# Kernel tuning notes

Hardware: AMD Instinct MI355X
Metric: run time of the kernel (lower is better)

The kernel has to match this reference:

```python
import jax, jax.numpy as jnp
import numpy as np

T = 4.0          # kd_T
PATCH_NUM = 16
MASK_NUM = 4
P = PATCH_NUM - MASK_NUM  # 12
B = 4096
D_IN = 640
D = 128


def embed(x, w1, b1, w2, b2):
    # Linear -> ReLU -> Linear -> L2 normalize over features
    h = jax.nn.relu(x @ w1.T + b1)
    y = h @ w2.T + b2
    norm = jnp.sqrt(jnp.sum(y * y, axis=1, keepdims=True))
    return y / norm


def kl_rows(y_s, y_t):
    # Matches KLDiv: kl_div(log_softmax(y_s/T), softmax(y_t/T), 'batchmean') * T^2
    # over dim=0 of a 1-D vector -> sum / D. Vectorized over leading dims.
    ls = jax.nn.log_softmax(y_s / T, axis=-1)
    lt = jax.nn.log_softmax(y_t / T, axis=-1)
    pt = jnp.exp(lt)
    return jnp.sum(pt * (lt - ls), axis=-1) / y_s.shape[-1] * (T * T)


def setup_inputs() -> dict:
    key = jax.random.key(0)
    ks = jax.random.split(key, 11)
    return {
        "ebg": jax.random.normal(ks[0], (B, D_IN), jnp.float32),
        "ebp": jax.random.normal(ks[1], (P * B, D_IN), jnp.float32),
        "labelsg": jax.random.randint(ks[2], (B,), 0, 64),
        "glo_w1": jax.random.normal(ks[3], (D, D_IN), jnp.float32) * 0.04,
        "glo_b1": jax.random.normal(ks[4], (D,), jnp.float32) * 0.02,
        "glo_w2": jax.random.normal(ks[5], (D, D), jnp.float32) * 0.09,
        "glo_b2": jax.random.normal(ks[6], (D,), jnp.float32) * 0.02,
        "pat_w1": jax.random.normal(ks[7], (D, D_IN), jnp.float32) * 0.04,
        "pat_b1": jax.random.normal(ks[8], (D,), jnp.float32) * 0.02,
        "pat_w2": jax.random.normal(ks[9], (D, D), jnp.float32) * 0.09,
        "pat_b2": jax.random.normal(ks[10], (D,), jnp.float32) * 0.02,
    }


def reference(ebg, ebp, labelsg, glo_w1, glo_b1, glo_w2, glo_b2,
              pat_w1, pat_b1, pat_w2, pat_b2):
    sg = jax.lax.stop_gradient
    g = embed(ebg, glo_w1, glo_b1, glo_w2, glo_b2)          # [B, D]
    p = embed(ebp, pat_w1, pat_b1, pat_w2, pat_b2)          # [P*B, D]
    p = p.reshape(P, B, D)
    p_bar = p.mean(axis=0)                                  # [B, D]

    # soft_dil_loss: symmetric KL between g[b] and p_bar[b]
    dil = jnp.sum(kl_rows(g, sg(p_bar)) + kl_rows(p_bar, sg(g)))

    # soft_dcl_loss: symmetric KL between (g[b]-p[b,l])^2 and (p_bar[b]-p[b,l])^2
    p_bt = jnp.transpose(p, (1, 0, 2))                      # [B, P, D]
    d1 = (g[:, None, :] - p_bt) ** 2                        # [B, P, D]
    d2 = (p_bar[:, None, :] - p_bt) ** 2                    # [B, P, D]
    dcl = jnp.sum(kl_rows(d1, sg(d2)) + kl_rows(d2, sg(d1))) / P

    return (dil, dcl)
```

## Files before the change

### kernel.cpp

```cpp
#include <hip/hip_runtime.h>
#include <math.h>

#define B_    4096
#define DIN   640
#define DD    128
#define PP    12
#define INV_T 0.25f

typedef __bf16 bft;
typedef __attribute__((ext_vector_type(8))) __bf16 bf16x8;
typedef __attribute__((ext_vector_type(4))) float fx4;

__device__ __forceinline__ void gload16(const float* gp, float* lp) {
  __builtin_amdgcn_global_load_lds(
      (const __attribute__((address_space(1))) unsigned int*)gp,
      (__attribute__((address_space(3))) unsigned int*)lp,
      16, 0, 0);
}

__global__ __launch_bounds__(256) void prep_kernel(
    const float* __restrict__ gw1, const float* __restrict__ pw1,
    const float* __restrict__ gw2, const float* __restrict__ pw2,
    bft* __restrict__ w1fg, bft* __restrict__ w1fp,
    bft* __restrict__ w2fg, bft* __restrict__ w2fp)
{
  int id = blockIdx.x * 256 + threadIdx.x;
  const float* src;
  bft* dst;
  int nt, kc, hl, lane, kstride;
  if (id < 40960) {
    const bool isg = (id < 20480);
    int f = isg ? id : (id - 20480);
    src = isg ? gw1 : pw1;
    dst = isg ? w1fg : w1fp;
    lane = f & 63;
    int q2 = f >> 6;
    hl = q2 & 1;
    int q3 = q2 >> 1;
    kc = q3 % 20; nt = q3 / 20;
    kstride = DIN;
    dst += ((size_t)(nt * 20 + kc) * 2 + hl) * 512 + lane * 8;
  } else {
    const bool isg = (id < 45056);
    int f = isg ? (id - 40960) : (id - 45056);
    src = isg ? gw2 : pw2;
    dst = isg ? w2fg : w2fp;
    lane = f & 63;
    int q2 = f >> 6;
    hl = q2 & 1;
    int q3 = q2 >> 1;
    kc = q3 & 3; nt = q3 >> 2;
    kstride = DD;
    dst += ((size_t)(nt * 4 + kc) * 2 + hl) * 512 + lane * 8;
  }
  int ln = lane & 15, quad = lane >> 4;
  const float* s = src + (size_t)(nt * 16 + ln) * kstride + kc * 32 + quad * 8;
#pragma unroll
  for (int e = 0; e < 8; e++) {
    float x = s[e];
    bft h = (bft)x;
    dst[e] = hl ? (bft)(x - (float)h) : h;
  }
}

__global__ __launch_bounds__(256, 2) void embed_kernel(
    const float* __restrict__ ebg, const float* __restrict__ ebp,
    const bft* __restrict__ w1fg, const float* __restrict__ b1g,
    const bft* __restrict__ w2fg, const float* __restrict__ b2g,
    const bft* __restrict__ w1fp, const float* __restrict__ b1p,
    const bft* __restrict__ w2fp, const float* __restrict__ b2p,
    float* __restrict__ outg, float* __restrict__ outp)
{
  __shared__ __align__(16) bft hsm[2 * 128 * 128];
  float* xbase = (float*)hsm;
  bft* hhi = hsm;
  bft* hlo = hsm + 128 * 128;
  float* halfsq = (float*)hsm;

  const int t = threadIdx.x;
  const int w = t >> 6, lane = t & 63;
  const int wm = w >> 1, wn = w & 1;
  const int ln = lane & 15, quad = lane >> 4;

  const float *X, *B1, *B2;
  const bft *W1F, *W2F;
  float* Y;
  long m0;
  const bool isg = (blockIdx.x < 32);
  if (isg) {
    X = ebg; W1F = w1fg; B1 = b1g; W2F = w2fg; B2 = b2g;
    Y = outg; m0 = (long)blockIdx.x * 128;
  } else {
    X = ebp; W1F = w1fp; B1 = b1p; W2F = w2fp; B2 = b2p;
    Y = outp; m0 = (long)(blockIdx.x - 32) * 128;
  }

  const int srow = lane >> 3;
  const int skq  = (lane & 7) ^ srow;
  const float* xsrc = X + (size_t)(m0 + w * 32 + srow) * DIN + skq * 4;
  const int ldst = w * 32 * 32 + lane * 4;

#define GLX(bufp, k0)                                        \
  _Pragma("unroll")                                          \
  for (int j = 0; j < 4; j++)                                \
    gload16(xsrc + (size_t)j * 8 * DIN + (k0), (bufp) + ldst + j * 8 * 32);

  const int s0 = ((quad << 1) ^ (ln & 7));

  const bft* p1f[4];
#pragma unroll
  for (int nt = 0; nt < 4; nt++)
    p1f[nt] = W1F + (size_t)(wn * 4 + nt) * 20480 + lane * 8;

  fx4 acc[4][4];
#pragma unroll
  for (int mt = 0; mt < 4; mt++)
#pragma unroll
    for (int nt = 0; nt < 4; nt++) acc[mt][nt] = (fx4){0.f, 0.f, 0.f, 0.f};

#define LOADW(wh, wl, kcv)                                 \
  _Pragma("unroll")                                        \
  for (int nt = 0; nt < 4; nt++) {                         \
    wh[nt] = *(const bf16x8*)(p1f[nt] + (kcv) * 1024);     \
    wl[nt] = *(const bf16x8*)(p1f[nt] + (kcv) * 1024 + 512); \
  }

#define PH1CHUNK(bufp, wh, wl)                                                         \
  {                                                                                    \
    bf16x8 ah[4], al[4];                                                               \
    _Pragma("unroll")                                                                  \
    for (int mt = 0; mt < 4; mt++) {                                                   \
      const float* rp = (bufp) + (wm * 64 + mt * 16 + ln) * 32;                        \
      fx4 x0 = *(const fx4*)(rp + s0 * 4);                                             \
      fx4 x1 = *(const fx4*)(rp + (s0 ^ 1) * 4);                                       \
      _Pragma("unroll")                                                                \
      for (int j = 0; j < 4; j++) {                                                    \
        float xv = x0[j];                                                              \
        bft hh = (bft)xv;                                                              \
        ah[mt][j] = hh;                                                                \
        al[mt][j] = (bft)(xv - (float)hh);                                             \
        float yv = x1[j];                                                              \
        bft hh2 = (bft)yv;                                                             \
        ah[mt][4 + j] = hh2;                                                           \
        al[mt][4 + j] = (bft)(yv - (float)hh2);                                        \
      }                                                                                \
    }                                                                                  \
    _Pragma("unroll")                                                                  \
    for (int mt = 0; mt < 4; mt++)                                                     \
      _Pragma("unroll")                                                                \
      for (int nt = 0; nt < 4; nt++) {                                                 \
        acc[mt][nt] = __builtin_amdgcn_mfma_f32_16x16x32_bf16(ah[mt], wh[nt], acc[mt][nt], 0, 0, 0); \
        acc[mt][nt] = __builtin_amdgcn_mfma_f32_16x16x32_bf16(al[mt], wh[nt], acc[mt][nt], 0, 0, 0); \
        acc[mt][nt] = __builtin_amdgcn_mfma_f32_16x16x32_bf16(ah[mt], wl[nt], acc[mt][nt], 0, 0, 0); \
      }                                                                                \
  }

  bf16x8 wha[4], wla[4], whb[4], wlb[4];
  GLX(xbase, 0)
  GLX(xbase + 4096, 32)
  GLX(xbase + 8192, 64)
  LOADW(wha, wla, 0)

#define HALFSTEP(c, WCH, WCL, WNH, WNL, VMTOK)                              \
  {                                                                          \
    const int kn_ = ((c) + 1 < 20) ? ((c) + 1) : 0;                          \
    LOADW(WNH, WNL, kn_)                                                     \
    asm volatile("s_waitcnt vmcnt(" VMTOK ") lgkmcnt(0)" ::: "memory");      \
    __builtin_amdgcn_s_barrier();                                            \
    __builtin_amdgcn_sched_barrier(0);                                       \
    const int kp_ = ((c) + 3 < 20) ? ((c) + 3) * 32 : 0;                     \
    float* pslot_ = xbase + ((((c) + 3) & 3) << 12);                         \
    GLX(pslot_, kp_)                                                         \
    PH1CHUNK(xbase + ((((c) & 3)) << 12), WCH, WCL)                          \
  }

  HALFSTEP(0, wha, wla, whb, wlb, "24")
  for (int kc = 1; kc < 19; kc += 2) {
    HALFSTEP(kc,     whb, wlb, wha, wla, "32")
    HALFSTEP(kc + 1, wha, wla, whb, wlb, "32")
  }
  HALFSTEP(19, whb, wlb, wha, wla, "32")

  __syncthreads();

#pragma unroll
  for (int nt = 0; nt < 4; nt++) {
    float bv = B1[wn * 64 + nt * 16 + ln];
    int c8 = wn * 8 + nt * 2 + (ln >> 3);
    int c7 = ln & 7;
#pragma unroll
    for (int mt = 0; mt < 4; mt++) {
#pragma unroll
      for (int r = 0; r < 4; r++) {
        float v = fmaxf(acc[mt][nt][r] + bv, 0.f);
        bft h = (bft)v;
        bft l = (bft)(v - (float)h);
        int m = wm * 64 + mt * 16 + quad * 4 + r;
        int addr = m * 128 + ((c8 ^ (m & 15)) << 3) + c7;
        hhi[addr] = h;
        hlo[addr] = l;
      }
    }
  }

  const bft* p2f[4];
#pragma unroll
  for (int nt = 0; nt < 4; nt++)
    p2f[nt] = W2F + (size_t)(wn * 4 + nt) * 4096 + lane * 8;

  fx4 acc2[4][4];
#pragma unroll
  for (int nt = 0; nt < 4; nt++) {
    float bv = B2[wn * 64 + nt * 16 + ln];
#pragma unroll
    for (int mt = 0; mt < 4; mt++) acc2[mt][nt] = (fx4){bv, bv, bv, bv};
  }

#define LOADW2(wh, wl, kcv)                                \
  _Pragma("unroll")                                        \
  for (int nt = 0; nt < 4; nt++) {                         \
    wh[nt] = *(const bf16x8*)(p2f[nt] + (kcv) * 1024);     \
    wl[nt] = *(const bf16x8*)(p2f[nt] + (kcv) * 1024 + 512); \
  }

#define PH2CHUNK(kcv, wh, wl)                                                          \
  {                                                                                    \
    bf16x8 ah2[4], al2[4];                                                             \
    _Pragma("unroll")                                                                  \
    for (int mt = 0; mt < 4; mt++) {                                                   \
      int m = wm * 64 + mt * 16 + ln;                                                  \
      int c8 = ((kcv) * 4 + quad) ^ (m & 15);                                          \
      ah2[mt] = *(const bf16x8*)&hhi[m * 128 + (c8 << 3)];                             \
      al2[mt] = *(const bf16x8*)&hlo[m * 128 + (c8 << 3)];                             \
    }                                                                                  \
    _Pragma("unroll")                                                                  \
    for (int mt = 0; mt < 4; mt++)                                                     \
      _Pragma("unroll")                                                                \
      for (int nt = 0; nt < 4; nt++) {                                                 \
        acc2[mt][nt] = __builtin_amdgcn_mfma_f32_16x16x32_bf16(ah2[mt], wh[nt], acc2[mt][nt], 0, 0, 0); \
        acc2[mt][nt] = __builtin_amdgcn_mfma_f32_16x16x32_bf16(al2[mt], wh[nt], acc2[mt][nt], 0, 0, 0); \
        acc2[mt][nt] = __builtin_amdgcn_mfma_f32_16x16x32_bf16(ah2[mt], wl[nt], acc2[mt][nt], 0, 0, 0); \
      }                                                                                \
  }

  bf16x8 q2ha[4], q2la[4], q2hb[4], q2lb[4];
  LOADW2(q2ha, q2la, 0)
  __syncthreads();
  LOADW2(q2hb, q2lb, 1)
  PH2CHUNK(0, q2ha, q2la)
  LOADW2(q2ha, q2la, 2)
  PH2CHUNK(1, q2hb, q2lb)
  LOADW2(q2hb, q2lb, 3)
  PH2CHUNK(2, q2ha, q2la)
  PH2CHUNK(3, q2hb, q2lb)
  __syncthreads();

#pragma unroll
  for (int mt = 0; mt < 4; mt++) {
#pragma unroll
    for (int r = 0; r < 4; r++) {
      float s = 0.f;
#pragma unroll
      for (int nt = 0; nt < 4; nt++) { float v = acc2[mt][nt][r]; s += v * v; }
      s += __shfl_xor(s, 1, 64);
      s += __shfl_xor(s, 2, 64);
      s += __shfl_xor(s, 4, 64);
      s += __shfl_xor(s, 8, 64);
      if (ln == 0) halfsq[(wm * 64 + mt * 16 + quad * 4 + r) * 2 + wn] = s;
    }
  }
  __syncthreads();
#pragma unroll
  for (int mt = 0; mt < 4; mt++) {
#pragma unroll
    for (int r = 0; r < 4; r++) {
      int row = wm * 64 + mt * 16 + quad * 4 + r;
      float rinv = 1.0f / sqrtf(halfsq[row * 2] + halfsq[row * 2 + 1]);
      long R = m0 + row;
#pragma unroll
      for (int nt = 0; nt < 4; nt++) {
        float val = acc2[mt][nt][r] * rinv;
        int col = wn * 64 + nt * 16 + ln;
        if (isg) {
          Y[R * DD + col] = val;
        } else {
          long l_ = R >> 12, b_ = R & 4095;
          Y[(b_ * PP + l_) * DD + col] = val;
        }
      }
    }
  }
}

__device__ __forceinline__ float sym_kl_row(float au0, float au1, float av0, float av1)
{
  float eu0 = __expf(au0), eu1 = __expf(au1);
  float ev0 = __expf(av0), ev1 = __expf(av1);
  float su = eu0 + eu1, sv = ev0 + ev1;
#pragma unroll
  for (int o = 32; o > 0; o >>= 1) {
    su += __shfl_xor(su, o, 64);
    sv += __shfl_xor(sv, o, 64);
  }
  float ru = 1.0f / su, rv = 1.0f / sv;
  float d0 = au0 - av0, d1 = au1 - av1;
  float part = (eu0 * ru - ev0 * rv) * d0 + (eu1 * ru - ev1 * rv) * d1;
#pragma unroll
  for (int o = 32; o > 0; o >>= 1) part += __shfl_xor(part, o, 64);
  return part;
}

__global__ __launch_bounds__(256) void loss_kernel(
    const float* __restrict__ g, const float* __restrict__ p,
    float* __restrict__ pdil, float* __restrict__ pdcl)
{
  __shared__ float wd[4], wc[4];
  int w = threadIdx.x >> 6, lane = threadIdx.x & 63;
  int b = blockIdx.x * 4 + w;
  float2 pl[PP];
  float sx = 0.f, sy = 0.f;
#pragma unroll
  for (int l = 0; l < PP; l++) {
    pl[l] = *(const float2*)&p[((size_t)b * PP + l) * DD + lane * 2];
    sx += pl[l].x; sy += pl[l].y;
  }
  sx *= (1.0f / PP); sy *= (1.0f / PP);
  float2 gv = *(const float2*)&g[(size_t)b * DD + lane * 2];

  float dil = sym_kl_row(gv.x * INV_T, gv.y * INV_T, sx * INV_T, sy * INV_T) * 0.125f;

  float dcl = 0.f;
#pragma unroll
  for (int l = 0; l < PP; l++) {
    float u0 = (gv.x - pl[l].x) * (gv.x - pl[l].x) * INV_T;
    float u1 = (gv.y - pl[l].y) * (gv.y - pl[l].y) * INV_T;
    float v0 = (sx - pl[l].x) * (sx - pl[l].x) * INV_T;
    float v1 = (sy - pl[l].y) * (sy - pl[l].y) * INV_T;
    dcl += sym_kl_row(u0, u1, v0, v1);
  }
  dcl *= (1.0f / 96.0f);

  if (lane == 0) { wd[w] = dil; wc[w] = dcl; }
  __syncthreads();
  if (threadIdx.x == 0) pdil[blockIdx.x] = wd[0] + wd[1] + wd[2] + wd[3];
  if (threadIdx.x == 1) pdcl[blockIdx.x] = wc[0] + wc[1] + wc[2] + wc[3];
}

__global__ __launch_bounds__(256) void final_kernel(const float* __restrict__ pdil,
                                                    const float* __restrict__ pdcl,
                                                    float* __restrict__ out)
{
  __shared__ float red[8];
  int t = threadIdx.x;
  float s0 = 0.f, s1 = 0.f;
  for (int i = t; i < 1024; i += 256) { s0 += pdil[i]; s1 += pdcl[i]; }
#pragma unroll
  for (int o = 32; o > 0; o >>= 1) {
    s0 += __shfl_xor(s0, o, 64);
    s1 += __shfl_xor(s1, o, 64);
  }
  int wid = t >> 6, lane = t & 63;
  if (lane == 0) { red[wid] = s0; red[4 + wid] = s1; }
  __syncthreads();
  if (t == 0) out[0] = red[0] + red[1] + red[2] + red[3];
  if (t == 1) out[1] = red[4] + red[5] + red[6] + red[7];
}

extern "C" void kernel_launch(void* const* d_in, const int* in_sizes, int n_in,
                              void* d_out, int out_size, void* d_ws, size_t ws_size,
                              hipStream_t stream)
{
  const float* ebg = (const float*)d_in[0];
  const float* ebp = (const float*)d_in[1];
  const float* gw1 = (const float*)d_in[3];
  const float* gb1 = (const float*)d_in[4];
  const float* gw2 = (const float*)d_in[5];
  const float* gb2 = (const float*)d_in[6];
  const float* pw1 = (const float*)d_in[7];
  const float* pb1 = (const float*)d_in[8];
  const float* pw2 = (const float*)d_in[9];
  const float* pb2 = (const float*)d_in[10];
  float* out = (float*)d_out;

  float* ws   = (float*)d_ws;
  float* g    = ws;
  float* p    = g + (size_t)B_ * DD;
  float* pdil = p + (size_t)PP * B_ * DD;
  float* pdcl = pdil + 1024;
  bft* wb   = (bft*)(pdcl + 1024);
  bft* w1fg = wb;
  bft* w1fp = w1fg + 163840;
  bft* w2fg = w1fp + 163840;
  bft* w2fp = w2fg + 32768;

  prep_kernel<<<192, 256, 0, stream>>>(gw1, pw1, gw2, pw2,
                                       w1fg, w1fp, w2fg, w2fp);
  embed_kernel<<<416, 256, 0, stream>>>(ebg, ebp,
                                        w1fg, gb1, w2fg, gb2,
                                        w1fp, pb1, w2fp, pb2,
                                        g, p);
  loss_kernel<<<B_ / 4, 256, 0, stream>>>(g, p, pdil, pdcl);
  final_kernel<<<1, 256, 0, stream>>>(pdil, pdcl, out);
}
```

Measured before the change: 246.0 us.

## Give each wave private X staging buffers to drop per-chunk block barriers

The phase-1 GEMM previously staged shared X tiles in a 4-slot ring and needed a workgroup s_barrier every k-chunk. Each wave now loads its own 64 rows into a private double-buffered LDS region, reads them into registers, and issues the next prefetch into the same slot, so only wave-local waitcnts are needed. This removes cross-wave synchronization, at the cost of duplicate X loads between the two wn waves sharing rows and shallower prefetch depth.

```diff
diff --git a/kernel.cpp b/kernel.cpp
--- a/kernel.cpp
+++ b/kernel.cpp
@@ -72,7 +72,7 @@
     float* __restrict__ outg, float* __restrict__ outp)
 {
   __shared__ __align__(16) bft hsm[2 * 128 * 128];
-  float* xbase = (float*)hsm;
+  float* xwave = (float*)hsm;
   bft* hhi = hsm;
   bft* hlo = hsm + 128 * 128;
   float* halfsq = (float*)hsm;
@@ -97,13 +97,13 @@
 
   const int srow = lane >> 3;
   const int skq  = (lane & 7) ^ srow;
-  const float* xsrc = X + (size_t)(m0 + w * 32 + srow) * DIN + skq * 4;
-  const int ldst = w * 32 * 32 + lane * 4;
-
-#define GLX(bufp, k0)                                        \
+  const float* xsrc = X + (size_t)(m0 + wm * 64 + srow) * DIN + skq * 4;
+  float* xw = xwave + w * 4096;
+
+#define GLX(slotp, k0)                                       \
   _Pragma("unroll")                                          \
-  for (int j = 0; j < 4; j++)                                \
-    gload16(xsrc + (size_t)j * 8 * DIN + (k0), (bufp) + ldst + j * 8 * 32);
+  for (int j = 0; j < 8; j++)                                \
+    gload16(xsrc + (size_t)j * 8 * DIN + (k0), (slotp) + lane * 4 + j * 256);
 
   const int s0 = ((quad << 1) ^ (ln & 7));
 
@@ -125,61 +125,63 @@
     wl[nt] = *(const bf16x8*)(p1f[nt] + (kcv) * 1024 + 512); \
   }
 
-#define PH1CHUNK(bufp, wh, wl)                                                         \
-  {                                                                                    \
-    bf16x8 ah[4], al[4];                                                               \
-    _Pragma("unroll")                                                                  \
-    for (int mt = 0; mt < 4; mt++) {                                                   \
-      const float* rp = (bufp) + (wm * 64 + mt * 16 + ln) * 32;                        \
-      fx4 x0 = *(const fx4*)(rp + s0 * 4);                                             \
-      fx4 x1 = *(const fx4*)(rp + (s0 ^ 1) * 4);                                       \
-      _Pragma("unroll")                                                                \
-      for (int j = 0; j < 4; j++) {                                                    \
-        float xv = x0[j];                                                              \
-        bft hh = (bft)xv;                                                              \
-        ah[mt][j] = hh;                                                                \
-        al[mt][j] = (bft)(xv - (float)hh);                                             \
-        float yv = x1[j];                                                              \
-        bft hh2 = (bft)yv;                                                             \
-        ah[mt][4 + j] = hh2;                                                           \
-        al[mt][4 + j] = (bft)(yv - (float)hh2);                                        \
-      }                                                                                \
-    }                                                                                  \
-    _Pragma("unroll")                                                                  \
-    for (int mt = 0; mt < 4; mt++)                                                     \
-      _Pragma("unroll")                                                                \
-      for (int nt = 0; nt < 4; nt++) {                                                 \
-        acc[mt][nt] = __builtin_amdgcn_mfma_f32_16x16x32_bf16(ah[mt], wh[nt], acc[mt][nt], 0, 0, 0); \
-        acc[mt][nt] = __builtin_amdgcn_mfma_f32_16x16x32_bf16(al[mt], wh[nt], acc[mt][nt], 0, 0, 0); \
-        acc[mt][nt] = __builtin_amdgcn_mfma_f32_16x16x32_bf16(ah[mt], wl[nt], acc[mt][nt], 0, 0, 0); \
-      }                                                                                \
-  }
-
-  bf16x8 wha[4], wla[4], whb[4], wlb[4];
-  GLX(xbase, 0)
-  GLX(xbase + 4096, 32)
-  GLX(xbase + 8192, 64)
-  LOADW(wha, wla, 0)
-
-#define HALFSTEP(c, WCH, WCL, WNH, WNL, VMTOK)                              \
+#define PH1STEP(c, WCH, WCL, WNH, WNL, VMTOK)                                \
   {                                                                          \
     const int kn_ = ((c) + 1 < 20) ? ((c) + 1) : 0;                          \
     LOADW(WNH, WNL, kn_)                                                     \
-    asm volatile("s_waitcnt vmcnt(" VMTOK ") lgkmcnt(0)" ::: "memory");      \
-    __builtin_amdgcn_s_barrier();                                            \
+    asm volatile("s_waitcnt vmcnt(" VMTOK ")" ::: "memory");                 \
     __builtin_amdgcn_sched_barrier(0);                                       \
-    const int kp_ = ((c) + 3 < 20) ? ((c) + 3) * 32 : 0;                     \
-    float* pslot_ = xbase + ((((c) + 3) & 3) << 12);                         \
-    GLX(pslot_, kp_)                                                         \
-    PH1CHUNK(xbase + ((((c) & 3)) << 12), WCH, WCL)                          \
-  }
-
-  HALFSTEP(0, wha, wla, whb, wlb, "24")
-  for (int kc = 1; kc < 19; kc += 2) {
-    HALFSTEP(kc,     whb, wlb, wha, wla, "32")
-    HALFSTEP(kc + 1, wha, wla, whb, wlb, "32")
-  }
-  HALFSTEP(19, whb, wlb, wha, wla, "32")
+    float* cur_ = xw + (((c) & 1) ? 2048 : 0);                               \
+    fx4 x0[4], x1[4];                                                        \
+    _Pragma("unroll")                                                        \
+    for (int mt = 0; mt < 4; mt++) {                                         \
+      const float* rp = cur_ + (mt * 16 + ln) * 32;                          \
+      x0[mt] = *(const fx4*)(rp + s0 * 4);                                   \
+      x1[mt] = *(const fx4*)(rp + (s0 ^ 1) * 4);                             \
+    }                                                                        \
+    asm volatile("s_waitcnt lgkmcnt(0)" ::: "memory");                       \
+    __builtin_amdgcn_sched_barrier(0);                                       \
+    const int kp_ = ((c) + 2 < 20) ? ((c) + 2) * 32 : 0;                     \
+    GLX(cur_, kp_)                                                           \
+    bf16x8 ah[4], al[4];                                                     \
+    _Pragma("unroll")                                                        \
+    for (int mt = 0; mt < 4; mt++) {                                         \
+      _Pragma("unroll")                                                      \
+      for (int j = 0; j < 4; j++) {                                          \
+        float xv = x0[mt][j];                                                \
+        bft hh = (bft)xv;                                                    \
+        ah[mt][j] = hh;                                                      \
+        al[mt][j] = (bft)(xv - (float)hh);                                   \
+        float yv = x1[mt][j];                                                \
+        bft hh2 = (bft)yv;                                                   \
+        ah[mt][4 + j] = hh2;                                                 \
+        al[mt][4 + j] = (bft)(yv - (float)hh2);                              \
+      }                                                                      \
+    }                                                                        \
+    _Pragma("unroll")                                                        \
+    for (int mt = 0; mt < 4; mt++)                                           \
+      _Pragma("unroll")                                                      \
+      for (int nt = 0; nt < 4; nt++) {                                       \
+        acc[mt][nt] = __builtin_amdgcn_mfma_f32_16x16x32_bf16(ah[mt], WCH[nt], acc[mt][nt], 0, 0, 0); \
+        acc[mt][nt] = __builtin_amdgcn_mfma_f32_16x16x32_bf16(al[mt], WCH[nt], acc[mt][nt], 0, 0, 0); \
+        acc[mt][nt] = __builtin_amdgcn_mfma_f32_16x16x32_bf16(ah[mt], WCL[nt], acc[mt][nt], 0, 0, 0); \
+      }                                                                      \
+  }
+
+  bf16x8 wha[4], wla[4], whb[4], wlb[4];
+  GLX(xw, 0)
+  GLX(xw + 2048, 32)
+  LOADW(wha, wla, 0)
+
+  PH1STEP(0, wha, wla, whb, wlb, "24")
+  PH1STEP(1, whb, wlb, wha, wla, "32")
+#pragma unroll 1
+  for (int kc = 2; kc < 18; kc += 2) {
+    PH1STEP(kc,     wha, wla, whb, wlb, "24")
+    PH1STEP(kc + 1, whb, wlb, wha, wla, "24")
+  }
+  PH1STEP(18, wha, wla, whb, wlb, "24")
+  PH1STEP(19, whb, wlb, wha, wla, "24")
 
   __syncthreads();
 
```

After: 255.6 us. +3.9%, slower.

## Restructure X staging into double-buffered 64-wide K chunks with one barrier pair per chunk

Applied to the files above, without the earlier changes.

Replaces the four-slot ring of 32-column X tiles, which needed one barrier per 32-column step, with two slots of 64-column tiles. Each step runs two MFMA halves and has one barrier before compute and one before refilling the slot. The swizzle and address math are redone for the 64-float row stride. This roughly halves barrier frequency per K. In exchange it has shallower prefetch depth, a rolled loop (unroll 1), and hand-tuned vmcnt values that must match the new load count.

```diff
diff --git a/kernel.cpp b/kernel.cpp
--- a/kernel.cpp
+++ b/kernel.cpp
@@ -95,17 +95,21 @@
     Y = outp; m0 = (long)(blockIdx.x - 32) * 128;
   }
 
-  const int srow = lane >> 3;
-  const int skq  = (lane & 7) ^ srow;
-  const float* xsrc = X + (size_t)(m0 + w * 32 + srow) * DIN + skq * 4;
-  const int ldst = w * 32 * 32 + lane * 4;
-
-#define GLX(bufp, k0)                                        \
+  const int q4 = lane >> 4;
+  int soff[8];
+#pragma unroll
+  for (int j = 0; j < 8; j++) {
+    int rl = w * 32 + j * 4 + q4;
+    int swz = (lane & 15) ^ (rl & 15);
+    soff[j] = rl * DIN + swz * 4;
+  }
+  const float* Xp = X + (size_t)m0 * DIN;
+  const int ldst = w * 2048 + lane * 4;
+
+#define GLX(slotp, k0)                                       \
   _Pragma("unroll")                                          \
-  for (int j = 0; j < 4; j++)                                \
-    gload16(xsrc + (size_t)j * 8 * DIN + (k0), (bufp) + ldst + j * 8 * 32);
-
-  const int s0 = ((quad << 1) ^ (ln & 7));
+  for (int j = 0; j < 8; j++)                                \
+    gload16(Xp + soff[j] + (k0), (slotp) + ldst + j * 256);
 
   const bft* p1f[4];
 #pragma unroll
@@ -125,14 +129,14 @@
     wl[nt] = *(const bf16x8*)(p1f[nt] + (kcv) * 1024 + 512); \
   }
 
-#define PH1CHUNK(bufp, wh, wl)                                                         \
+#define PH1HALF(slotp, K8, wh, wl)                                                     \
   {                                                                                    \
     bf16x8 ah[4], al[4];                                                               \
     _Pragma("unroll")                                                                  \
     for (int mt = 0; mt < 4; mt++) {                                                   \
-      const float* rp = (bufp) + (wm * 64 + mt * 16 + ln) * 32;                        \
-      fx4 x0 = *(const fx4*)(rp + s0 * 4);                                             \
-      fx4 x1 = *(const fx4*)(rp + (s0 ^ 1) * 4);                                       \
+      const float* rp = (slotp) + (wm * 64 + mt * 16 + ln) * 64;                       \
+      fx4 x0 = *(const fx4*)(rp + ((((K8) + (quad << 1))     ^ ln) << 2));             \
+      fx4 x1 = *(const fx4*)(rp + ((((K8) + (quad << 1) + 1) ^ ln) << 2));             \
       _Pragma("unroll")                                                                \
       for (int j = 0; j < 4; j++) {                                                    \
         float xv = x0[j];                                                              \
@@ -155,31 +159,36 @@
       }                                                                                \
   }
 
-  bf16x8 wha[4], wla[4], whb[4], wlb[4];
-  GLX(xbase, 0)
-  GLX(xbase + 4096, 32)
-  GLX(xbase + 8192, 64)
-  LOADW(wha, wla, 0)
-
-#define HALFSTEP(c, WCH, WCL, WNH, WNL, VMTOK)                              \
+#define EMBSTEP(c_, VMTOK)                                                   \
   {                                                                          \
-    const int kn_ = ((c) + 1 < 20) ? ((c) + 1) : 0;                          \
-    LOADW(WNH, WNL, kn_)                                                     \
+    const int kn_ = (2 * (c_) + 1 < 20) ? 2 * (c_) + 1 : 0;                  \
+    LOADW(whb, wlb, kn_)                                                     \
     asm volatile("s_waitcnt vmcnt(" VMTOK ") lgkmcnt(0)" ::: "memory");      \
     __builtin_amdgcn_s_barrier();                                            \
     __builtin_amdgcn_sched_barrier(0);                                       \
-    const int kp_ = ((c) + 3 < 20) ? ((c) + 3) * 32 : 0;                     \
-    float* pslot_ = xbase + ((((c) + 3) & 3) << 12);                         \
-    GLX(pslot_, kp_)                                                         \
-    PH1CHUNK(xbase + ((((c) & 3)) << 12), WCH, WCL)                          \
-  }
-
-  HALFSTEP(0, wha, wla, whb, wlb, "24")
-  for (int kc = 1; kc < 19; kc += 2) {
-    HALFSTEP(kc,     whb, wlb, wha, wla, "32")
-    HALFSTEP(kc + 1, wha, wla, whb, wlb, "32")
-  }
-  HALFSTEP(19, whb, wlb, wha, wla, "32")
+    float* slot_ = xbase + (((c_) & 1) << 13);                               \
+    PH1HALF(slot_, 0, wha, wla)                                              \
+    const int knn_ = (2 * (c_) + 2 < 20) ? 2 * (c_) + 2 : 0;                 \
+    LOADW(wha, wla, knn_)                                                    \
+    PH1HALF(slot_, 8, whb, wlb)                                              \
+    asm volatile("s_waitcnt lgkmcnt(0)" ::: "memory");                       \
+    __builtin_amdgcn_s_barrier();                                            \
+    __builtin_amdgcn_sched_barrier(0);                                       \
+    const int kp_ = ((c_) + 2 < 10) ? ((c_) + 2) * 64 : 0;                   \
+    GLX(slot_, kp_)                                                          \
+  }
+
+  bf16x8 wha[4], wla[4], whb[4], wlb[4];
+  GLX(xbase, 0)
+  GLX(xbase + 8192, 64)
+  LOADW(wha, wla, 0)
+
+  EMBSTEP(0, "32")
+  EMBSTEP(1, "48")
+#pragma unroll 1
+  for (int c = 2; c < 10; c++) {
+    EMBSTEP(c, "40")
+  }
 
   __syncthreads();
 
```

Result: no change. 248.8 us (+1.2%).
